# Kernel tuning notes

Measured on AMD Instinct MI355X. Metric: run time of the kernel, lower is better.

## Reference

```python
import jax, jax.numpy as jnp
import numpy as np

DIM = 128      # token feature dim
HEADS = 4
HEAD_DIM = DIM // HEADS
H = 512
W = 512
NSP = 4096     # n_spixels = H*W/scale
TEMP = DIM ** (-0.5)   # NOTE: original scales by full-dim ** -0.5
NEG = -9.0e15
EPS = 1e-12    # torch F.normalize eps


def setup_inputs() -> dict:
    key = jax.random.key(0)
    k1, k2, k3, k4 = jax.random.split(key, 4)
    return {
        "spf": jax.random.normal(k1, (DIM, NSP), jnp.float32),
        "segments": jax.random.randint(k2, (H, W), 0, NSP, jnp.int32),
        "w_qkv": jax.random.normal(k3, (DIM, 3 * DIM), jnp.float32) / np.sqrt(DIM),
        "w_out": jax.random.normal(k4, (DIM, DIM), jnp.float32) / np.sqrt(DIM),
        "b_out": jnp.zeros((DIM,), jnp.float32),
    }


def build_adjacency(seg, n_sp):
    """Vectorized version of get_A: for every 2x2 window (i in [0,h-3], j in [0,w-3])
    connect the max and min superpixel labels; zero the diagonal."""
    a = seg[:-2, :-2]
    b = seg[:-2, 1:-1]
    c = seg[1:-1, :-2]
    d = seg[1:-1, 1:-1]
    mx = jnp.maximum(jnp.maximum(a, b), jnp.maximum(c, d)).ravel()
    mn = jnp.minimum(jnp.minimum(a, b), jnp.minimum(c, d)).ravel()
    A = jnp.zeros((n_sp, n_sp), jnp.float32)
    A = A.at[mx, mn].set(1.0)
    A = A.at[mn, mx].set(1.0)
    # fill_diagonal(A, 0) (also removes windows where max == min)
    A = A * (1.0 - jnp.eye(n_sp, dtype=jnp.float32))
    return A


def _l2norm(t):
    n = jnp.sqrt(jnp.sum(t * t, axis=-1, keepdims=True))
    return t / jnp.maximum(n, EPS)


def reference(spf, segments, w_qkv, w_out, b_out):
    A = build_adjacency(segments, NSP)                      # [n, n]
    x = spf.T                                               # [n, dim]
    qkv = x @ w_qkv                                         # [n, 3*dim]
    q, k, v = jnp.split(qkv, 3, axis=-1)
    split = lambda t: t.reshape(NSP, HEADS, HEAD_DIM).transpose(1, 0, 2)  # [h, n, d]
    q, k, v = split(q), split(k), split(v)
    q = _l2norm(q)
    k = _l2norm(k)
    # Original masks per-head scores, then keeps only head 0's attention
    # (attn[0][0]) and broadcasts it over all heads' v. We compute only
    # head 0's scores (mathematically identical output).
    scores = (q[0] @ k[0].T) * TEMP                         # [n, n] cosine scores
    scores = jnp.where(A > 0, scores, NEG)
    eye = jnp.eye(NSP, dtype=bool)
    scores = jnp.where(eye, 1.0, scores)                    # np.fill_diagonal(attn, 1)
    attn = jax.nn.softmax(scores, axis=-1)                  # [n, n]
    out = jnp.einsum('nm,hmd->hnd', attn, v)                # shared attn over heads
    out = out.transpose(1, 0, 2).reshape(NSP, DIM)          # [n, dim]
    out = out @ w_out + b_out                               # to_out Linear
    # map_sp2p: scatter superpixel features back to pixel grid (hard assignment)
    pix = out[segments]                                     # [H, W, dim]
    return pix.transpose(2, 0, 1)[None]                     # [1, dim, H, W]
```

## Files before the change

kernel.cpp:

```cpp
#include <hip/hip_runtime.h>

#define NSP 4096
#define HW 512
#define TEMP 0.08838834764831845f
#define MAXE 640
#define PREP_ZERO 512
#define PREP_WF 64
#define ADJ_BLOCKS 1017
#define QKV_BLOCKS 768

__global__ void __launch_bounds__(256) prep(
    unsigned int* __restrict__ mask, const float* __restrict__ wqkv,
    const float* __restrict__ wout, float* __restrict__ Wf) {
    int t = threadIdx.x;
    if (blockIdx.x < PREP_ZERO) {
        ((uint4*)mask)[blockIdx.x * 256 + t] = make_uint4(0u, 0u, 0u, 0u);
        return;
    }
    int gid = (blockIdx.x - PREP_ZERO) * 256 + t;
    int d = gid >> 7, c = gid & 127;
    float acc = 0.f;
#pragma unroll 8
    for (int k = 0; k < 128; ++k)
        acc += wqkv[d * 384 + 256 + k] * wout[k * 128 + c];
    Wf[d * 128 + c] = acc;
}

__global__ void __launch_bounds__(256) adj_qkv(
    const int* __restrict__ seg, unsigned int* __restrict__ mask,
    const float* __restrict__ spf, const float* __restrict__ wqkv,
    const float* __restrict__ Wf,
    float* __restrict__ Q0, float* __restrict__ K0, float* __restrict__ V) {
    int t = threadIdx.x;
    if (blockIdx.x < ADJ_BLOCKS) {
        int idx = blockIdx.x * 256 + t;
        if (idx >= 510 * 510) return;
        int i = idx / 510, j = idx - i * 510;
        const int* r = seg + i * HW + j;
        int a = r[0], b = r[1], c = r[HW], d = r[HW + 1];
        int mx = max(max(a, b), max(c, d));
        int mn = min(min(a, b), min(c, d));
        if (mx == mn) return;
        atomicOr(&mask[mx * 128 + (mn >> 5)], 1u << (mn & 31));
        atomicOr(&mask[mn * 128 + (mx >> 5)], 1u << (mx & 31));
        return;
    }
    int gid = (blockIdx.x - ADJ_BLOCKS) * 256 + t;
    int g = gid % 48;
    int n = gid / 48;
    const float* wbase;
    int wstride;
    float* outp;
    if (g < 8)       { wbase = wqkv + g * 4;               wstride = 384; outp = Q0 + n * 32  + g * 4; }
    else if (g < 16) { wbase = wqkv + 128 + (g - 8) * 4;   wstride = 384; outp = K0 + n * 32  + (g - 8) * 4; }
    else             { wbase = Wf + (g - 16) * 4;          wstride = 128; outp = V  + n * 128 + (g - 16) * 4; }
    float4 acc = {0.f, 0.f, 0.f, 0.f};
#pragma unroll 8
    for (int d = 0; d < 128; ++d) {
        float x = spf[d * NSP + n];
        float4 w = *(const float4*)(wbase + d * wstride);
        acc.x += x * w.x; acc.y += x * w.y; acc.z += x * w.z; acc.w += x * w.w;
    }
    if (g < 16) {
        float s = acc.x * acc.x + acc.y * acc.y + acc.z * acc.z + acc.w * acc.w;
        s += __shfl_xor(s, 1);
        s += __shfl_xor(s, 2);
        s += __shfl_xor(s, 4);
        float inv = 1.0f / fmaxf(sqrtf(s), 1e-12f);
        acc.x *= inv; acc.y *= inv; acc.z *= inv; acc.w *= inv;
    }
    *(float4*)outp = acc;
}

__global__ void __launch_bounds__(128) sparse_attn(
    const unsigned int* __restrict__ mask, const float* __restrict__ Q0,
    const float* __restrict__ K0, const float* __restrict__ V,
    const float* __restrict__ bout, float* __restrict__ final) {
    int n = blockIdx.x;
    int t = threadIdx.x;
    int lane = t & 63, wid = t >> 6;
    __shared__ unsigned int words[128];
    __shared__ int   pfx[128];
    __shared__ int   midx[MAXE];
    __shared__ float wts[MAXE];
    __shared__ float q0s[32];
    __shared__ float4 redv[4][32];
    __shared__ float  redw[4];

    unsigned int w = mask[n * 128 + t];
    words[t] = w;
    if (t < 32) q0s[t] = Q0[n * 32 + t];

    int p = __popc(w);
#pragma unroll
    for (int off = 1; off < 64; off <<= 1) {
        int y = __shfl_up(p, off);
        if (lane >= off) p += y;
    }
    pfx[t] = p;
    __syncthreads();
    if (wid == 1) pfx[t] = p + pfx[63];
    __syncthreads();
    int E = min(pfx[127], MAXE);

    for (int e = t; e < E; e += 128) {
        int lo = 0, hi = 127;
        while (lo < hi) { int mid = (lo + hi) >> 1; if (pfx[mid] > e) hi = mid; else lo = mid + 1; }
        int base = (lo > 0) ? pfx[lo - 1] : 0;
        int r = e - base;
        unsigned int x = words[lo];
        for (int i = 0; i < r; ++i) x &= x - 1;
        int m = lo * 32 + (__ffs(x) - 1);
        const float4* kp = (const float4*)(K0 + m * 32);
        float s = 0.f;
#pragma unroll
        for (int i = 0; i < 8; ++i) {
            float4 kv = kp[i];
            s += q0s[i * 4 + 0] * kv.x + q0s[i * 4 + 1] * kv.y +
                 q0s[i * 4 + 2] * kv.z + q0s[i * 4 + 3] * kv.w;
        }
        wts[e]  = __expf(s * TEMP - 1.0f);
        midx[e] = m;
    }
    __syncthreads();

    int cg = t & 31, eg = t >> 5;
    const float4* V4 = (const float4*)V;
    float4 acc = {0.f, 0.f, 0.f, 0.f};
    float wp = 0.f;
    int e = eg;
    for (; e + 4 < E; e += 8) {
        float wa = wts[e];     int ma = midx[e];
        float wb = wts[e + 4]; int mb = midx[e + 4];
        float4 va = V4[ma * 32 + cg];
        float4 vb = V4[mb * 32 + cg];
        acc.x += wa * va.x + wb * vb.x;
        acc.y += wa * va.y + wb * vb.y;
        acc.z += wa * va.z + wb * vb.z;
        acc.w += wa * va.w + wb * vb.w;
        wp += wa + wb;
    }
    for (; e < E; e += 4) {
        float wt = wts[e];
        float4 v = V4[midx[e] * 32 + cg];
        acc.x += wt * v.x; acc.y += wt * v.y; acc.z += wt * v.z; acc.w += wt * v.w;
        wp += wt;
    }
    redv[eg][cg] = acc;
    if (cg == 0) redw[eg] = wp;
    __syncthreads();
    if (t < 32) {
        float4 a0 = redv[0][t], a1 = redv[1][t], a2 = redv[2][t], a3 = redv[3][t];
        float ws = 1.0f + redw[0] + redw[1] + redw[2] + redw[3];
        float4 vd = V4[n * 32 + t];
        float4 bb = ((const float4*)bout)[t];
        float inv = 1.0f / ws;
        float4 o;
        o.x = (a0.x + a1.x + a2.x + a3.x + vd.x) * inv + bb.x;
        o.y = (a0.y + a1.y + a2.y + a3.y + vd.y) * inv + bb.y;
        o.z = (a0.z + a1.z + a2.z + a3.z + vd.z) * inv + bb.z;
        o.w = (a0.w + a1.w + a2.w + a3.w + vd.w) * inv + bb.w;
        ((float4*)final)[n * 32 + t] = o;
    }
}

#define GOUT_PIX 256
#define GOUT_CH  32
__global__ void __launch_bounds__(256) gather_out(
    const float* __restrict__ final, const int* __restrict__ seg,
    float* __restrict__ out) {
    __shared__ __align__(16) float tile[GOUT_CH][260];
    __shared__ int sseg[GOUT_PIX];
    int t = threadIdx.x;
    int pixbase = (blockIdx.x >> 2) * GOUT_PIX;
    int cbase = (blockIdx.x & 3) * GOUT_CH;

    sseg[t] = seg[pixbase + t];
    __syncthreads();

    const float4* f4 = (const float4*)final;
    int c8 = t & 7;
    int pp = t >> 3;
#pragma unroll
    for (int i = 0; i < 8; ++i) {
        int p = pp + 32 * i;
        float4 v = f4[sseg[p] * 32 + (cbase >> 2) + c8];
        tile[4 * c8 + 0][p] = v.x;
        tile[4 * c8 + 1][p] = v.y;
        tile[4 * c8 + 2][p] = v.z;
        tile[4 * c8 + 3][p] = v.w;
    }
    __syncthreads();

    int wv = t >> 6, lane = t & 63;
#pragma unroll
    for (int s = 0; s < 8; ++s) {
        int ch = wv * 8 + s;
        float4 v = *(const float4*)&tile[ch][4 * lane];
        *(float4*)(out + (size_t)(cbase + ch) * (HW * HW) + pixbase + 4 * lane) = v;
    }
}

extern "C" void kernel_launch(void* const* d_in, const int* in_sizes, int n_in,
                              void* d_out, int out_size, void* d_ws, size_t ws_size,
                              hipStream_t stream) {
    const float* spf  = (const float*)d_in[0];
    const int*   seg  = (const int*)d_in[1];
    const float* wqkv = (const float*)d_in[2];
    const float* wout = (const float*)d_in[3];
    const float* bout = (const float*)d_in[4];
    float* out = (float*)d_out;

    char* ws = (char*)d_ws;
    unsigned int* mask = (unsigned int*)ws;
    float* Q0    = (float*)(ws + (2u << 20));
    float* K0    = (float*)(ws + (2u << 20) + (512u << 10));
    float* V     = (float*)(ws + (3u << 20));
    float* final = (float*)(ws + (5u << 20));
    float* Wf    = (float*)(ws + (7u << 20));

    hipLaunchKernelGGL(prep, dim3(PREP_ZERO + PREP_WF), dim3(256), 0, stream,
                       mask, wqkv, wout, Wf);
    hipLaunchKernelGGL(adj_qkv, dim3(ADJ_BLOCKS + QKV_BLOCKS), dim3(256), 0, stream,
                       seg, mask, spf, wqkv, Wf, Q0, K0, V);
    hipLaunchKernelGGL(sparse_attn, dim3(4096), dim3(128), 0, stream,
                       mask, Q0, K0, V, bout, final);
    hipLaunchKernelGGL(gather_out, dim3((HW * HW / GOUT_PIX) * 4), dim3(256), 0, stream,
                       final, seg, out);
}
```

Baseline: 211.7 us.

## Build neighbor lists during adjacency and tile QKV projection through shared memory

During adjacency construction, the returned value of the atomicOr is checked, and each newly set edge is appended to a per-row neighbor list using an atomic counter. The attention kernel then reads these lists directly and no longer rebuilds them from the bitmask with a prefix scan, binary search and bit stripping. The QKV projection is also restructured: each block stages 16 tokens of input in shared memory and every thread computes Q or K plus two V chunks, so there are fewer blocks and the input is reused. The price is extra atomics, scattered neighbor stores, and neighbor order that varies between runs, so floating-point summation order is no longer deterministic.

```diff
diff --git a/kernel.cpp b/kernel.cpp
--- a/kernel.cpp
+++ b/kernel.cpp
@@ -4,17 +4,17 @@
 #define HW 512
 #define TEMP 0.08838834764831845f
 #define MAXE 640
-#define PREP_ZERO 512
+#define PREP_ZERO 516
 #define PREP_WF 64
 #define ADJ_BLOCKS 1017
-#define QKV_BLOCKS 768
+#define GEMM_BLOCKS 256
 
 __global__ void __launch_bounds__(256) prep(
-    unsigned int* __restrict__ mask, const float* __restrict__ wqkv,
+    unsigned int* __restrict__ zero_base, const float* __restrict__ wqkv,
     const float* __restrict__ wout, float* __restrict__ Wf) {
     int t = threadIdx.x;
     if (blockIdx.x < PREP_ZERO) {
-        ((uint4*)mask)[blockIdx.x * 256 + t] = make_uint4(0u, 0u, 0u, 0u);
+        ((uint4*)zero_base)[blockIdx.x * 256 + t] = make_uint4(0u, 0u, 0u, 0u);
         return;
     }
     int gid = (blockIdx.x - PREP_ZERO) * 256 + t;
@@ -28,6 +28,7 @@
 
 __global__ void __launch_bounds__(256) adj_qkv(
     const int* __restrict__ seg, unsigned int* __restrict__ mask,
+    int* __restrict__ cnt, int* __restrict__ nbr,
     const float* __restrict__ spf, const float* __restrict__ wqkv,
     const float* __restrict__ Wf,
     float* __restrict__ Q0, float* __restrict__ K0, float* __restrict__ V) {
@@ -41,76 +42,78 @@
         int mx = max(max(a, b), max(c, d));
         int mn = min(min(a, b), min(c, d));
         if (mx == mn) return;
-        atomicOr(&mask[mx * 128 + (mn >> 5)], 1u << (mn & 31));
-        atomicOr(&mask[mn * 128 + (mx >> 5)], 1u << (mx & 31));
+        unsigned int o1 = atomicOr(&mask[mx * 128 + (mn >> 5)], 1u << (mn & 31));
+        if (!((o1 >> (mn & 31)) & 1u)) {
+            int s = atomicAdd(&cnt[mx], 1);
+            if (s < MAXE) nbr[mx * MAXE + s] = mn;
+        }
+        unsigned int o2 = atomicOr(&mask[mn * 128 + (mx >> 5)], 1u << (mx & 31));
+        if (!((o2 >> (mx & 31)) & 1u)) {
+            int s = atomicAdd(&cnt[mn], 1);
+            if (s < MAXE) nbr[mn * MAXE + s] = mx;
+        }
         return;
     }
-    int gid = (blockIdx.x - ADJ_BLOCKS) * 256 + t;
-    int g = gid % 48;
-    int n = gid / 48;
-    const float* wbase;
-    int wstride;
-    float* outp;
-    if (g < 8)       { wbase = wqkv + g * 4;               wstride = 384; outp = Q0 + n * 32  + g * 4; }
-    else if (g < 16) { wbase = wqkv + 128 + (g - 8) * 4;   wstride = 384; outp = K0 + n * 32  + (g - 8) * 4; }
-    else             { wbase = Wf + (g - 16) * 4;          wstride = 128; outp = V  + n * 128 + (g - 16) * 4; }
-    float4 acc = {0.f, 0.f, 0.f, 0.f};
-#pragma unroll 8
+    __shared__ float xs[128][16];
+    int nbase = (blockIdx.x - ADJ_BLOCKS) * 16;
+#pragma unroll
+    for (int i = 0; i < 8; ++i) {
+        int idx = t + 256 * i;
+        int d = idx >> 4, nn = idx & 15;
+        xs[d][nn] = spf[d * NSP + nbase + nn];
+    }
+    __syncthreads();
+    int n = t >> 4, k = t & 15;
+    int nglob = nbase + n;
+    const float* wq = (k < 8) ? (wqkv + k * 4) : (wqkv + 96 + k * 4);
+    const float* wv1 = Wf + k * 4;
+    const float* wv2 = Wf + 64 + k * 4;
+    float4 a0 = {0.f, 0.f, 0.f, 0.f};
+    float4 a1 = {0.f, 0.f, 0.f, 0.f};
+    float4 a2 = {0.f, 0.f, 0.f, 0.f};
+#pragma unroll 4
     for (int d = 0; d < 128; ++d) {
-        float x = spf[d * NSP + n];
-        float4 w = *(const float4*)(wbase + d * wstride);
-        acc.x += x * w.x; acc.y += x * w.y; acc.z += x * w.z; acc.w += x * w.w;
-    }
-    if (g < 16) {
-        float s = acc.x * acc.x + acc.y * acc.y + acc.z * acc.z + acc.w * acc.w;
-        s += __shfl_xor(s, 1);
-        s += __shfl_xor(s, 2);
-        s += __shfl_xor(s, 4);
-        float inv = 1.0f / fmaxf(sqrtf(s), 1e-12f);
-        acc.x *= inv; acc.y *= inv; acc.z *= inv; acc.w *= inv;
-    }
-    *(float4*)outp = acc;
+        float x = xs[d][n];
+        float4 wa = *(const float4*)(wq + d * 384);
+        float4 wb = *(const float4*)(wv1 + d * 128);
+        float4 wc = *(const float4*)(wv2 + d * 128);
+        a0.x += x * wa.x; a0.y += x * wa.y; a0.z += x * wa.z; a0.w += x * wa.w;
+        a1.x += x * wb.x; a1.y += x * wb.y; a1.z += x * wb.z; a1.w += x * wb.w;
+        a2.x += x * wc.x; a2.y += x * wc.y; a2.z += x * wc.z; a2.w += x * wc.w;
+    }
+    float s = a0.x * a0.x + a0.y * a0.y + a0.z * a0.z + a0.w * a0.w;
+    s += __shfl_xor(s, 1);
+    s += __shfl_xor(s, 2);
+    s += __shfl_xor(s, 4);
+    float inv = 1.0f / fmaxf(sqrtf(s), 1e-12f);
+    a0.x *= inv; a0.y *= inv; a0.z *= inv; a0.w *= inv;
+    float* qk = (k < 8) ? (Q0 + nglob * 32 + k * 4) : (K0 + nglob * 32 + (k - 8) * 4);
+    *(float4*)qk = a0;
+    *(float4*)(V + nglob * 128 + k * 4) = a1;
+    *(float4*)(V + nglob * 128 + 64 + k * 4) = a2;
 }
 
 __global__ void __launch_bounds__(128) sparse_attn(
-    const unsigned int* __restrict__ mask, const float* __restrict__ Q0,
-    const float* __restrict__ K0, const float* __restrict__ V,
-    const float* __restrict__ bout, float* __restrict__ final) {
+    const int* __restrict__ cnt, const int* __restrict__ nbr,
+    const float* __restrict__ Q0, const float* __restrict__ K0,
+    const float* __restrict__ V, const float* __restrict__ bout,
+    float* __restrict__ final) {
     int n = blockIdx.x;
     int t = threadIdx.x;
-    int lane = t & 63, wid = t >> 6;
-    __shared__ unsigned int words[128];
-    __shared__ int   pfx[128];
     __shared__ int   midx[MAXE];
     __shared__ float wts[MAXE];
     __shared__ float q0s[32];
     __shared__ float4 redv[4][32];
     __shared__ float  redw[4];
-
-    unsigned int w = mask[n * 128 + t];
-    words[t] = w;
+    __shared__ int sE;
+
     if (t < 32) q0s[t] = Q0[n * 32 + t];
-
-    int p = __popc(w);
-#pragma unroll
-    for (int off = 1; off < 64; off <<= 1) {
-        int y = __shfl_up(p, off);
-        if (lane >= off) p += y;
-    }
-    pfx[t] = p;
-    __syncthreads();
-    if (wid == 1) pfx[t] = p + pfx[63];
-    __syncthreads();
-    int E = min(pfx[127], MAXE);
+    if (t == 0) sE = min(cnt[n], MAXE);
+    __syncthreads();
+    int E = sE;
 
     for (int e = t; e < E; e += 128) {
-        int lo = 0, hi = 127;
-        while (lo < hi) { int mid = (lo + hi) >> 1; if (pfx[mid] > e) hi = mid; else lo = mid + 1; }
-        int base = (lo > 0) ? pfx[lo - 1] : 0;
-        int r = e - base;
-        unsigned int x = words[lo];
-        for (int i = 0; i < r; ++i) x &= x - 1;
-        int m = lo * 32 + (__ffs(x) - 1);
+        int m = nbr[n * MAXE + e];
         const float4* kp = (const float4*)(K0 + m * 32);
         float s = 0.f;
 #pragma unroll
@@ -213,18 +216,20 @@
 
     char* ws = (char*)d_ws;
     unsigned int* mask = (unsigned int*)ws;
-    float* Q0    = (float*)(ws + (2u << 20));
-    float* K0    = (float*)(ws + (2u << 20) + (512u << 10));
-    float* V     = (float*)(ws + (3u << 20));
-    float* final = (float*)(ws + (5u << 20));
-    float* Wf    = (float*)(ws + (7u << 20));
+    int*   cnt   = (int*)(ws + 0x200000);
+    float* Q0    = (float*)(ws + 0x210000);
+    float* K0    = (float*)(ws + 0x290000);
+    float* V     = (float*)(ws + 0x310000);
+    float* final = (float*)(ws + 0x510000);
+    float* Wf    = (float*)(ws + 0x710000);
+    int*   nbr   = (int*)(ws + 0x720000);
 
     hipLaunchKernelGGL(prep, dim3(PREP_ZERO + PREP_WF), dim3(256), 0, stream,
                        mask, wqkv, wout, Wf);
-    hipLaunchKernelGGL(adj_qkv, dim3(ADJ_BLOCKS + QKV_BLOCKS), dim3(256), 0, stream,
-                       seg, mask, spf, wqkv, Wf, Q0, K0, V);
+    hipLaunchKernelGGL(adj_qkv, dim3(ADJ_BLOCKS + GEMM_BLOCKS), dim3(256), 0, stream,
+                       seg, mask, cnt, nbr, spf, wqkv, Wf, Q0, K0, V);
     hipLaunchKernelGGL(sparse_attn, dim3(4096), dim3(128), 0, stream,
-                       mask, Q0, K0, V, bout, final);
+                       cnt, nbr, Q0, K0, V, bout, final);
     hipLaunchKernelGGL(gather_out, dim3((HW * HW / GOUT_PIX) * 4), dim3(256), 0, stream,
                        final, seg, out);
 }
```

New measurement: 294.8 us. +39.3%, slower.
